# Kernel optimization log

Hardware: AMD Instinct MI355X
Metric: run time of the kernel (lower is better)

Reference implementation:

```python
import jax, jax.numpy as jnp
import numpy as np

EMBED_DIM = 1024
NUM_HEADS = 16
HEAD_DIM = EMBED_DIM // NUM_HEADS

# Hamilton-product combination tensor C[out_comp, weight_comp, in_comp]
_C = np.zeros((4, 4, 4), dtype=np.float32)
for o, terms in enumerate([
    [(0, 0, 1), (1, 1, -1), (2, 2, -1), (3, 3, -1)],  # r_out
    [(1, 0, 1), (0, 1, 1), (3, 2, 1), (2, 3, -1)],    # i_out
    [(2, 0, 1), (3, 1, -1), (0, 2, 1), (1, 3, 1)],    # j_out
    [(3, 0, 1), (2, 1, 1), (1, 2, -1), (0, 3, 1)],    # k_out
]):
    for d, c, s in terms:
        _C[o, d, c] = s
C = jnp.asarray(_C)


def _xavier(key, shape):
    fan_in, fan_out = shape[-1], shape[-2]
    a = jnp.sqrt(6.0 / (fan_in + fan_out))
    return jax.random.uniform(key, shape, jnp.float32, -a, a)


def setup_inputs() -> dict:
    key = jax.random.key(0)
    ks = jax.random.split(key, 8)
    B, T, E = 4, 1024, EMBED_DIM
    inp = {
        'q': jax.random.normal(ks[0], (B, T, E, 4), jnp.float32),
        'k': jax.random.normal(ks[1], (B, T, E, 4), jnp.float32),
        'v': jax.random.normal(ks[2], (B, T, E, 4), jnp.float32),
    }
    for name, kk in zip(['Wq', 'Wk', 'Wv', 'Wo'], ks[3:7]):
        # stacked [r,i,j,k] weights, each (out_features, in_features)
        inp[name] = _xavier(kk, (4, E, E))
        inp[name.replace('W', 'b')] = jnp.zeros((E, 4), jnp.float32)
    return inp


def qlinear(x, W, b):
    # x: [B,T,in,4(c)], W: [4(d),out,in], b: [out,4]
    # effective block weight: Weff[q_out, c_in, out, in]
    Weff = jnp.einsum('doi,qdc->qcoi', W, C)
    out = jnp.einsum('btic,qcoi->btoq', x, Weff)
    return out + b  # bias broadcasts over B,T


def split_heads(x):
    B, T, D, Q = x.shape
    x = x.reshape(B, T, NUM_HEADS, HEAD_DIM, Q)
    return x.transpose(0, 2, 1, 3, 4)  # [B,H,T,hd,4]


def combine_heads(x):
    B, H, T, D, Q = x.shape
    return x.transpose(0, 2, 1, 3, 4).reshape(B, T, H * D, Q)


def reference(q, k, v, Wq, bq, Wk, bk, Wv, bv, Wo, bo):
    qh = split_heads(qlinear(q, Wq, bq))
    kh = split_heads(qlinear(k, Wk, bk))
    vh = split_heads(qlinear(v, Wv, bv))
    scale = 1.0 / jnp.sqrt(jnp.float32(HEAD_DIM * 4))
    scores = jnp.einsum('bhqfd,bhkfd->bhqk', qh, kh) * scale
    attn = jax.nn.softmax(scores, axis=-1)
    out = jnp.einsum('bhqk,bhkfd->bhqfd', attn, vh)
    return qlinear(combine_heads(out), Wo, bo)
```

## Files before the change

kernel.cpp:

```cpp
#include <hip/hip_runtime.h>
#include <hip/hip_bf16.h>

typedef _Float16 h16;
typedef h16   h16x8 __attribute__((ext_vector_type(8)));
typedef h16   h16x4 __attribute__((ext_vector_type(4)));
typedef float f32x4 __attribute__((ext_vector_type(4)));

#define EMB 1024
#define ED4 4096L

__device__ __forceinline__ void gload_lds16(const void* g, void* l) {
    __builtin_amdgcn_global_load_lds(
        (__attribute__((address_space(1))) void*)g,
        (__attribute__((address_space(3))) void*)l,
        16, 0, 0);
}

__global__ __launch_bounds__(256) void k_build_m(const float* __restrict__ W, h16* __restrict__ M) {
    int t = blockIdx.x * 256 + threadIdx.x;
    int i = t & 1023;
    int n = t >> 10;
    int o = n >> 2, q = n & 3;
    unsigned packed = 0xEu | (0x8u << 4) | (0x2u << 8) | (0x4u << 12);
    unsigned sm = (packed >> (q * 4)) & 0xFu;
    h16x4 out;
#pragma unroll
    for (int c = 0; c < 4; ++c) {
        int d = q ^ c;
        float w = W[((long)d * EMB + o) * EMB + i];
        out[c] = (h16)(((sm >> c) & 1u) ? -w : w);
    }
    *(h16x4*)&M[(long)n * ED4 + i * 4] = out;
}

__global__ __launch_bounds__(256) void k_f32_to_f16(const float* __restrict__ in, h16* __restrict__ out) {
    long i = ((long)blockIdx.x * 256 + threadIdx.x) * 4;
    float4 v = *(const float4*)(in + i);
    h16x4 o;
    o[0] = (h16)v.x; o[1] = (h16)v.y; o[2] = (h16)v.z; o[3] = (h16)v.w;
    *(h16x4*)(out + i) = o;
}

#define BAR() __builtin_amdgcn_s_barrier()
#define LGKM0() do { asm volatile("s_waitcnt lgkmcnt(0)" ::: "memory"); \
                     __builtin_amdgcn_sched_barrier(0); } while (0)
#define STAGE(matv, basev, row0v, tt, hh) do { \
    const h16* _src = (basev) + ((row0v) + (hh) * 128L) * 4096L + (long)(tt) * 64 + scol; \
    h16* _dst = &lds[(((tt) & 1) << 15) + (matv) * 16384 + (hh) * 8192 + w * 512]; \
    gload_lds16(_src, _dst); \
    gload_lds16(_src + 64 * 4096L, _dst + 4096); \
} while (0)
#define LDA_(mh, m, ks) (*(const h16x8*)&lds[cb + (mh) * 8192 + (wm * 64 + (m) * 16 + fr) * 64 + ((((ks) * 4 + kq) ^ fr7) << 3)])
#define LDB_(nh, n, ks) (*(const h16x8*)&lds[cb + 16384 + (nh) * 8192 + (wn * 32 + (n) * 16 + fr) * 64 + ((((ks) * 4 + kq) ^ fr7) << 3)])
#define MFMA_Q(MH, NH, BF) do { \
    __builtin_amdgcn_s_setprio(1); \
    _Pragma("unroll") \
    for (int m = 0; m < 4; ++m) \
        _Pragma("unroll") \
        for (int n = 0; n < 2; ++n) { \
            acc[MH][NH][m][n] = __builtin_amdgcn_mfma_f32_16x16x32_f16(af[m][0], BF[n][0], acc[MH][NH][m][n], 0, 0, 0); \
            acc[MH][NH][m][n] = __builtin_amdgcn_mfma_f32_16x16x32_f16(af[m][1], BF[n][1], acc[MH][NH][m][n], 0, 0, 0); \
        } \
    __builtin_amdgcn_s_setprio(0); \
} while (0)

template <typename OUT_T>
__global__ __launch_bounds__(512, 2) void k_gemm256(
    const h16* __restrict__ A, const h16* __restrict__ B,
    OUT_T* __restrict__ C, const float* __restrict__ bias, int nt)
{
    __shared__ __align__(16) h16 lds[65536];

    const int tid = threadIdx.x;
    const int w  = tid >> 6, l = tid & 63;
    const int wm = w >> 2, wn = w & 3;
    const int fr = l & 15, fr7 = l & 7, kq = l >> 4;

    const int srow = w * 8 + (l >> 3);
    const int scol = ((l & 7) ^ ((l >> 3) & 7)) << 3;
    const long arow0 = (long)blockIdx.x * 256 + srow;
    const long brow0 = (long)blockIdx.y * 256 + srow;

    f32x4 acc[2][2][4][2] = {};

    STAGE(0, A, arow0, 0, 0);
    STAGE(1, B, brow0, 0, 0);
    STAGE(0, A, arow0, 0, 1);
    STAGE(1, B, brow0, 0, 1);
    STAGE(0, A, arow0, 1, 0);
    STAGE(1, B, brow0, 1, 0);
    asm volatile("s_waitcnt vmcnt(4)" ::: "memory");
    __builtin_amdgcn_sched_barrier(0);
    BAR();

    for (int t = 0; t < nt; ++t) {
        const int cb = (t & 1) << 15;
        h16x8 af[4][2], b0[2][2], b1[2][2];

#pragma unroll
        for (int m = 0; m < 4; ++m) { af[m][0] = LDA_(0, m, 0); af[m][1] = LDA_(0, m, 1); }
#pragma unroll
        for (int n = 0; n < 2; ++n) { b0[n][0] = LDB_(0, n, 0); b0[n][1] = LDB_(0, n, 1); }
        if (t + 1 < nt) STAGE(0, A, arow0, t + 1, 1);
        BAR(); LGKM0();
        MFMA_Q(0, 0, b0);
        BAR();

#pragma unroll
        for (int n = 0; n < 2; ++n) { b1[n][0] = LDB_(1, n, 0); b1[n][1] = LDB_(1, n, 1); }
        if (t + 1 < nt) STAGE(1, B, brow0, t + 1, 1);
        BAR(); LGKM0();
        MFMA_Q(0, 1, b1);
        BAR();

#pragma unroll
        for (int m = 0; m < 4; ++m) { af[m][0] = LDA_(1, m, 0); af[m][1] = LDA_(1, m, 1); }
        if (t + 2 < nt) STAGE(0, A, arow0, t + 2, 0);
        BAR(); LGKM0();
        MFMA_Q(1, 0, b0);
        BAR();

        if (t + 2 < nt) STAGE(1, B, brow0, t + 2, 0);
        if (t < nt - 2) { asm volatile("s_waitcnt vmcnt(4)" ::: "memory"); }
        else            { asm volatile("s_waitcnt vmcnt(0)" ::: "memory"); }
        __builtin_amdgcn_sched_barrier(0);
        BAR();
        MFMA_Q(1, 1, b1);
        BAR();
    }

    const long row00 = (long)blockIdx.x * 256 + wm * 64 + kq * 4;
    const int  col00 = (int)blockIdx.y * 256 + wn * 32 + fr;
#pragma unroll
    for (int mh = 0; mh < 2; ++mh)
#pragma unroll
        for (int nh = 0; nh < 2; ++nh)
#pragma unroll
            for (int n = 0; n < 2; ++n) {
                const int col = col00 + nh * 128 + n * 16;
                const float bv = bias[col];
#pragma unroll
                for (int m = 0; m < 4; ++m) {
                    const long r0 = row00 + mh * 128 + m * 16;
#pragma unroll
                    for (int j = 0; j < 4; ++j)
                        C[(r0 + j) * 4096L + col] = (OUT_T)(acc[mh][nh][m][n][j] + bv);
                }
            }
}

template <typename OUT_T, bool HAS_BIAS>
__global__ __launch_bounds__(256) void k_gemm_bt(
    const h16* __restrict__ A, const h16* __restrict__ B,
    OUT_T* __restrict__ C, const float* __restrict__ bias,
    int lda, int ldb, int ldc,
    long sAb, long sAh, long sBb, long sBh, long sCb, long sCh,
    float alpha, int kIters)
{
    __shared__ __align__(16) h16 As[128 * 32];
    __shared__ __align__(16) h16 Bs[128 * 32];

    const int z = blockIdx.z, zb = z >> 4, zh = z & 15;
    const h16* Ab = A + zb * sAb + zh * sAh + (long)blockIdx.x * 128 * lda;
    const h16* Bb = B + zb * sBb + zh * sBh + (long)blockIdx.y * 128 * ldb;

    const int tid = threadIdx.x, w = tid >> 6, lane = tid & 63;
    const int wr = (w >> 1) * 64, wc = (w & 1) * 64;
    const int scol = (((lane & 3) ^ ((lane >> 3) & 3)) * 8);
    const int srow = lane >> 2;
    const int fr   = lane & 15;
    const int koff = (((lane >> 4) ^ ((fr >> 1) & 3)) * 8);

    f32x4 acc[4][4] = {};

    for (int kt = 0; kt < kIters; ++kt) {
        const int k0 = kt * 32;
#pragma unroll
        for (int j = 0; j < 2; ++j) {
            const int ca  = w * 2 + j;
            const int row = ca * 16 + srow;
            gload_lds16(Ab + (long)row * lda + k0 + scol, &As[ca * 512]);
            gload_lds16(Bb + (long)row * ldb + k0 + scol, &Bs[ca * 512]);
        }
        __syncthreads();

        h16x8 af[4], bfr[4];
#pragma unroll
        for (int m = 0; m < 4; ++m)
            af[m] = *(const h16x8*)&As[(wr + m * 16 + fr) * 32 + koff];
#pragma unroll
        for (int n = 0; n < 4; ++n)
            bfr[n] = *(const h16x8*)&Bs[(wc + n * 16 + fr) * 32 + koff];
        __syncthreads();

#pragma unroll
        for (int m = 0; m < 4; ++m)
#pragma unroll
            for (int n = 0; n < 4; ++n)
                acc[m][n] = __builtin_amdgcn_mfma_f32_16x16x32_f16(af[m], bfr[n], acc[m][n], 0, 0, 0);
    }

    OUT_T* Cb = C + zb * sCb + zh * sCh;
    const long rbase = (long)blockIdx.x * 128 + wr + (lane >> 4) * 4;
    const int  cbase = blockIdx.y * 128 + wc + fr;
#pragma unroll
    for (int n = 0; n < 4; ++n) {
        const int col = cbase + n * 16;
        const float bv = HAS_BIAS ? bias[col] : 0.0f;
#pragma unroll
        for (int m = 0; m < 4; ++m) {
            const long row0 = rbase + m * 16;
#pragma unroll
            for (int j = 0; j < 4; ++j) {
                float vv = acc[m][n][j] * alpha + bv;
                Cb[(row0 + j) * ldc + col] = (OUT_T)vv;
            }
        }
    }
}

__global__ void k_transpose_v(const h16* __restrict__ Vb, h16* __restrict__ Vt) {
    __shared__ h16 tile[32][34];
    const int z = blockIdx.z, b = z >> 4, h = z & 15;
    const int f0 = blockIdx.x * 32, t0 = blockIdx.y * 32;
    const int tx = threadIdx.x, ty = threadIdx.y;
#pragma unroll
    for (int j = 0; j < 4; ++j)
        tile[ty + 8 * j][tx] = Vb[(long)(b * 1024 + t0 + ty + 8 * j) * ED4 + h * 256 + f0 + tx];
    __syncthreads();
#pragma unroll
    for (int j = 0; j < 4; ++j)
        Vt[(long)z * (256 * 1024) + (long)(f0 + ty + 8 * j) * 1024 + t0 + tx] = tile[tx][ty + 8 * j];
}

__global__ __launch_bounds__(256) void k_softmax(h16* __restrict__ S) {
    const long row = blockIdx.x;
    h16* p = S + row * 1024;
    const int tid = threadIdx.x, w = tid >> 6, lane = tid & 63;
    h16x4 xi = *(const h16x4*)&p[tid * 4];
    float x[4];
#pragma unroll
    for (int j = 0; j < 4; ++j) x[j] = (float)xi[j];
    float m = fmaxf(fmaxf(x[0], x[1]), fmaxf(x[2], x[3]));
#pragma unroll
    for (int off = 32; off; off >>= 1) m = fmaxf(m, __shfl_xor(m, off));
    __shared__ float red[8];
    if (lane == 0) red[w] = m;
    __syncthreads();
    m = fmaxf(fmaxf(red[0], red[1]), fmaxf(red[2], red[3]));
    float s = 0.0f;
#pragma unroll
    for (int j = 0; j < 4; ++j) { x[j] = __expf(x[j] - m); s += x[j]; }
#pragma unroll
    for (int off = 32; off; off >>= 1) s += __shfl_xor(s, off);
    if (lane == 0) red[4 + w] = s;
    __syncthreads();
    s = red[4] + red[5] + red[6] + red[7];
    const float inv = 1.0f / s;
    h16x4 o;
#pragma unroll
    for (int j = 0; j < 4; ++j) o[j] = (h16)(x[j] * inv);
    *(h16x4*)&p[tid * 4] = o;
}

extern "C" void kernel_launch(void* const* d_in, const int* in_sizes, int n_in,
                              void* d_out, int out_size, void* d_ws, size_t ws_size,
                              hipStream_t stream) {
    const float* q  = (const float*)d_in[0];
    const float* k  = (const float*)d_in[1];
    const float* v  = (const float*)d_in[2];
    const float* Wq = (const float*)d_in[3];
    const float* bq = (const float*)d_in[4];
    const float* Wk = (const float*)d_in[5];
    const float* bk = (const float*)d_in[6];
    const float* Wv = (const float*)d_in[7];
    const float* bv = (const float*)d_in[8];
    const float* Wo = (const float*)d_in[9];
    const float* bo = (const float*)d_in[10];
    float* out = (float*)d_out;

    char* ws = (char*)d_ws;
    const long MB = 1024L * 1024;
    h16* X  = (h16*)(ws + 0 * MB);
    h16* M  = (h16*)(ws + 32 * MB);
    h16* Qb = (h16*)(ws + 64 * MB);
    h16* Kb = (h16*)(ws + 96 * MB);
    h16* Vb = (h16*)(ws + 128 * MB);
    h16* Vt = (h16*)(ws + 160 * MB);
    h16* AO = (h16*)(ws + 192 * MB);
    h16* Sc = (h16*)(ws + 224 * MB);

    dim3 blk(256);
    dim3 g256(16, 16, 1);

    k_f32_to_f16<<<16384, blk, 0, stream>>>(q, X);
    k_build_m<<<16384, blk, 0, stream>>>(Wq, M);
    k_gemm256<h16><<<g256, 512, 0, stream>>>(X, M, Qb, bq, 64);

    k_f32_to_f16<<<16384, blk, 0, stream>>>(k, X);
    k_build_m<<<16384, blk, 0, stream>>>(Wk, M);
    k_gemm256<h16><<<g256, 512, 0, stream>>>(X, M, Kb, bk, 64);

    k_f32_to_f16<<<16384, blk, 0, stream>>>(v, X);
    k_build_m<<<16384, blk, 0, stream>>>(Wv, M);
    k_gemm256<h16><<<g256, 512, 0, stream>>>(X, M, Vb, bv, 64);

    k_transpose_v<<<dim3(8, 32, 64), dim3(32, 8), 0, stream>>>(Vb, Vt);

    for (int c = 0; c < 4; ++c) {
        const h16* Qc  = Qb + (long)c * 1024 * 4096;
        const h16* Kc  = Kb + (long)c * 1024 * 4096;
        const h16* VtC = Vt + (long)c * 16 * 256 * 1024;
        h16*       AOc = AO + (long)c * 1024 * 4096;

        k_gemm_bt<h16, false><<<dim3(8, 8, 16), blk, 0, stream>>>(
            Qc, Kc, Sc, nullptr,
            4096, 4096, 1024,
            0, 256,
            0, 256,
            0, 1024L * 1024,
            0.0625f, 8);

        k_softmax<<<16384, blk, 0, stream>>>(Sc);

        k_gemm_bt<h16, false><<<dim3(8, 2, 16), blk, 0, stream>>>(
            Sc, VtC, AOc, nullptr,
            1024, 1024, 4096,
            0, 1024L * 1024,
            0, 256L * 1024,
            0, 256,
            1.0f, 32);
    }

    k_build_m<<<16384, blk, 0, stream>>>(Wo, M);
    k_gemm256<float><<<g256, 512, 0, stream>>>(AO, M, out, bo, 64);
}
```

Baseline: 906.7 us.

## Fuse V transpose into projection GEMM epilogue and trim main-loop barriers

The V projection GEMM gets a template flag that makes its epilogue write results straight into the per-head transposed Vt layout, as packed 4-wide half vectors. This removes the separate transpose kernel and its extra read and write of the V buffer. The GEMM main loop also drops several workgroup barriers, relying on the remaining post-MFMA barriers and the waitcnts for LDS ordering. The trade-off is that the transposed epilogue stores are strided and less coalesced. The lighter synchronisation depends on the remaining barriers still covering the double-buffer hazards.

Result: faster. 874.4 us (-3.6%).

```diff
diff --git a/kernel.cpp b/kernel.cpp
--- a/kernel.cpp
+++ b/kernel.cpp
@@ -64,7 +64,7 @@
     __builtin_amdgcn_s_setprio(0); \
 } while (0)
 
-template <typename OUT_T>
+template <typename OUT_T, bool VT>
 __global__ __launch_bounds__(512, 2) void k_gemm256(
     const h16* __restrict__ A, const h16* __restrict__ B,
     OUT_T* __restrict__ C, const float* __restrict__ bias, int nt)
@@ -102,21 +102,21 @@
 #pragma unroll
         for (int n = 0; n < 2; ++n) { b0[n][0] = LDB_(0, n, 0); b0[n][1] = LDB_(0, n, 1); }
         if (t + 1 < nt) STAGE(0, A, arow0, t + 1, 1);
-        BAR(); LGKM0();
+        LGKM0();
         MFMA_Q(0, 0, b0);
         BAR();
 
 #pragma unroll
         for (int n = 0; n < 2; ++n) { b1[n][0] = LDB_(1, n, 0); b1[n][1] = LDB_(1, n, 1); }
         if (t + 1 < nt) STAGE(1, B, brow0, t + 1, 1);
-        BAR(); LGKM0();
+        LGKM0();
         MFMA_Q(0, 1, b1);
         BAR();
 
 #pragma unroll
         for (int m = 0; m < 4; ++m) { af[m][0] = LDA_(1, m, 0); af[m][1] = LDA_(1, m, 1); }
         if (t + 2 < nt) STAGE(0, A, arow0, t + 2, 0);
-        BAR(); LGKM0();
+        LGKM0();
         MFMA_Q(1, 0, b0);
         BAR();
 
@@ -124,7 +124,6 @@
         if (t < nt - 2) { asm volatile("s_waitcnt vmcnt(4)" ::: "memory"); }
         else            { asm volatile("s_waitcnt vmcnt(0)" ::: "memory"); }
         __builtin_amdgcn_sched_barrier(0);
-        BAR();
         MFMA_Q(1, 1, b1);
         BAR();
     }
@@ -142,9 +141,17 @@
 #pragma unroll
                 for (int m = 0; m < 4; ++m) {
                     const long r0 = row00 + mh * 128 + m * 16;
-#pragma unroll
-                    for (int j = 0; j < 4; ++j)
-                        C[(r0 + j) * 4096L + col] = (OUT_T)(acc[mh][nh][m][n][j] + bv);
+                    if constexpr (VT) {
+                        h16x4 o;
+#pragma unroll
+                        for (int j = 0; j < 4; ++j) o[j] = (h16)(acc[mh][nh][m][n][j] + bv);
+                        const long zidx = (r0 >> 10) * 16 + (col >> 8);
+                        *(h16x4*)((h16*)C + zidx * 262144L + (long)(col & 255) * 1024 + (r0 & 1023)) = o;
+                    } else {
+#pragma unroll
+                        for (int j = 0; j < 4; ++j)
+                            C[(r0 + j) * 4096L + col] = (OUT_T)(acc[mh][nh][m][n][j] + bv);
+                    }
                 }
             }
 }
@@ -217,20 +224,6 @@
             }
         }
     }
-}
-
-__global__ void k_transpose_v(const h16* __restrict__ Vb, h16* __restrict__ Vt) {
-    __shared__ h16 tile[32][34];
-    const int z = blockIdx.z, b = z >> 4, h = z & 15;
-    const int f0 = blockIdx.x * 32, t0 = blockIdx.y * 32;
-    const int tx = threadIdx.x, ty = threadIdx.y;
-#pragma unroll
-    for (int j = 0; j < 4; ++j)
-        tile[ty + 8 * j][tx] = Vb[(long)(b * 1024 + t0 + ty + 8 * j) * ED4 + h * 256 + f0 + tx];
-    __syncthreads();
-#pragma unroll
-    for (int j = 0; j < 4; ++j)
-        Vt[(long)z * (256 * 1024) + (long)(f0 + ty + 8 * j) * 1024 + t0 + tx] = tile[tx][ty + 8 * j];
 }
 
 __global__ __launch_bounds__(256) void k_softmax(h16* __restrict__ S) {
@@ -285,27 +278,24 @@
     h16* M  = (h16*)(ws + 32 * MB);
     h16* Qb = (h16*)(ws + 64 * MB);
     h16* Kb = (h16*)(ws + 96 * MB);
-    h16* Vb = (h16*)(ws + 128 * MB);
-    h16* Vt = (h16*)(ws + 160 * MB);
-    h16* AO = (h16*)(ws + 192 * MB);
-    h16* Sc = (h16*)(ws + 224 * MB);
+    h16* Vt = (h16*)(ws + 128 * MB);
+    h16* AO = (h16*)(ws + 160 * MB);
+    h16* Sc = (h16*)(ws + 192 * MB);
 
     dim3 blk(256);
     dim3 g256(16, 16, 1);
 
     k_f32_to_f16<<<16384, blk, 0, stream>>>(q, X);
     k_build_m<<<16384, blk, 0, stream>>>(Wq, M);
-    k_gemm256<h16><<<g256, 512, 0, stream>>>(X, M, Qb, bq, 64);
+    k_gemm256<h16, false><<<g256, 512, 0, stream>>>(X, M, Qb, bq, 64);
 
     k_f32_to_f16<<<16384, blk, 0, stream>>>(k, X);
     k_build_m<<<16384, blk, 0, stream>>>(Wk, M);
-    k_gemm256<h16><<<g256, 512, 0, stream>>>(X, M, Kb, bk, 64);
+    k_gemm256<h16, false><<<g256, 512, 0, stream>>>(X, M, Kb, bk, 64);
 
     k_f32_to_f16<<<16384, blk, 0, stream>>>(v, X);
     k_build_m<<<16384, blk, 0, stream>>>(Wv, M);
-    k_gemm256<h16><<<g256, 512, 0, stream>>>(X, M, Vb, bv, 64);
-
-    k_transpose_v<<<dim3(8, 32, 64), dim3(32, 8), 0, stream>>>(Vb, Vt);
+    k_gemm256<h16, true><<<g256, 512, 0, stream>>>(X, M, Vt, bv, 64);
 
     for (int c = 0; c < 4; ++c) {
         const h16* Qc  = Qb + (long)c * 1024 * 4096;
@@ -333,5 +323,5 @@
     }
 
     k_build_m<<<16384, blk, 0, stream>>>(Wo, M);
-    k_gemm256<float><<<g256, 512, 0, stream>>>(AO, M, out, bo, 64);
-}
+    k_gemm256<float, false><<<g256, 512, 0, stream>>>(AO, M, out, bo, 64);
+}
```
